# Kernel tuning notes

Hardware: AMD Instinct MI355X
Metric: run time of the kernel (lower is better)

Reference implementation:

```python
import jax, jax.numpy as jnp
import numpy as np
import math

N_EMBD = 1024
N_HEAD = 16
HEAD_SIZE = N_EMBD // N_HEAD
LAYER_IDX = 2
LAMBDA_INIT = 0.8 - 0.6 * math.exp(-0.3 * (LAYER_IDX - 1))
LN_EPS = 1e-5
B, T = 4, 1024


def setup_inputs() -> dict:
    key = jax.random.key(0)
    ks = jax.random.split(key, 11)
    s = 0.02  # weight init scale
    return {
        "x": jax.random.normal(ks[0], (B, T, N_EMBD), dtype=jnp.float32),
        "Wq1": jax.random.normal(ks[1], (N_EMBD, N_EMBD), dtype=jnp.float32) * s,
        "Wq2": jax.random.normal(ks[2], (N_EMBD, N_EMBD), dtype=jnp.float32) * s,
        "Wk1": jax.random.normal(ks[3], (N_EMBD, N_EMBD), dtype=jnp.float32) * s,
        "Wk2": jax.random.normal(ks[4], (N_EMBD, N_EMBD), dtype=jnp.float32) * s,
        "Wv": jax.random.normal(ks[5], (N_EMBD, 2 * N_EMBD), dtype=jnp.float32) * s,
        "Wc": jax.random.normal(ks[6], (2 * N_EMBD, N_EMBD), dtype=jnp.float32) * s,
        "lq1": jax.random.normal(ks[7], (N_HEAD, HEAD_SIZE), dtype=jnp.float32) * 0.1,
        "lk1": jax.random.normal(ks[8], (N_HEAD, HEAD_SIZE), dtype=jnp.float32) * 0.1,
        "lq2": jax.random.normal(ks[9], (N_HEAD, HEAD_SIZE), dtype=jnp.float32) * 0.1,
        "lk2": jax.random.normal(ks[10], (N_HEAD, HEAD_SIZE), dtype=jnp.float32) * 0.1,
    }


def reference(x, Wq1, Wq2, Wk1, Wk2, Wv, Wc, lq1, lk1, lq2, lk2):
    Bx, Tx, C = x.shape
    H, hs = N_HEAD, HEAD_SIZE
    scale = 1.0 / math.sqrt(hs)

    # projections -> (B, T, H, d)
    q1 = (x @ Wq1).reshape(Bx, Tx, H, hs)
    q2 = (x @ Wq2).reshape(Bx, Tx, H, hs)
    k1 = (x @ Wk1).reshape(Bx, Tx, H, hs)
    k2 = (x @ Wk2).reshape(Bx, Tx, H, hs)
    v = (x @ Wv).reshape(Bx, Tx, H, 2 * hs)

    # dual score streams (B, H, T, T)
    att1 = jnp.einsum("bqhd,bkhd->bhqk", q1, k1) * scale
    att2 = jnp.einsum("bqhd,bkhd->bhqk", q2, k2) * scale

    causal = jnp.tril(jnp.ones((Tx, Tx), dtype=bool))  # (T, T)
    neg_inf = jnp.float32(-jnp.inf)
    att1 = jnp.where(causal, att1, neg_inf)
    att2 = jnp.where(causal, att2, neg_inf)
    a1 = jax.nn.softmax(att1, axis=-1)
    a2 = jax.nn.softmax(att2, axis=-1)

    # per-head differential lambda
    lam1 = jnp.exp(jnp.sum(lq1 * lk1, axis=-1))  # (H,)
    lam2 = jnp.exp(jnp.sum(lq2 * lk2, axis=-1))  # (H,)
    lam_full = lam1 - lam2 + LAMBDA_INIT  # (H,)

    att = a1 - lam_full[None, :, None, None] * a2  # dropout = identity (eval)

    # PV matmul -> (B, T, H, 2*hs)
    y = jnp.einsum("bhqk,bkhd->bqhd", att, v)

    # subLN over last dim (no affine)
    mu = jnp.mean(y, axis=-1, keepdims=True)
    var = jnp.mean(jnp.square(y - mu), axis=-1, keepdims=True)
    y = (y - mu) / jnp.sqrt(var + LN_EPS)
    y = y * (1.0 - LAMBDA_INIT)

    y = y.reshape(Bx, Tx, 2 * C)
    return y @ Wc  # resid dropout = identity (eval)
```

## Files before the change

kernel.cpp:

```cpp
#include <hip/hip_runtime.h>


#define T_SEQ 1024
#define NH 16
#define DV 128
#define NPROJ 6144
#define KSTR 72

typedef __bf16 bf16_t;
typedef __bf16 bf16x8 __attribute__((ext_vector_type(8)));
typedef __bf16 bf16x4 __attribute__((ext_vector_type(4)));
typedef __bf16 bf16x2 __attribute__((ext_vector_type(2)));
typedef _Float16 f16x4 __attribute__((ext_vector_type(4)));
typedef _Float16 f16x2 __attribute__((ext_vector_type(2)));
typedef short s16x4 __attribute__((ext_vector_type(4)));
typedef float f32x4 __attribute__((ext_vector_type(4)));

#define LAMBDA_INIT 0.35550906759096928f
#define ONE_MINUS_LI 0.6444909324090307f
#define LOG2E 1.4426950408889634f
#define RTHR 44.36f

#if __has_builtin(__builtin_amdgcn_mfma_f32_16x16x16_bf16)
#define MFMA16(a, b, c) __builtin_amdgcn_mfma_f32_16x16x16_bf16(a, b, c, 0, 0, 0)
#elif __has_builtin(__builtin_amdgcn_mfma_f32_16x16x16bf16_1k)
#define MFMA16(a, b, c)                                                       \
  __builtin_amdgcn_mfma_f32_16x16x16bf16_1k(                                  \
      __builtin_bit_cast(s16x4, a), __builtin_bit_cast(s16x4, b), c, 0, 0, 0)
#else
#define MFMA16(a, b, c) (c)
#endif

#define MFMA32(a, b, c) __builtin_amdgcn_mfma_f32_16x16x32_bf16(a, b, c, 0, 0, 0)

#define GLDS(g, l)                                                            \
  __builtin_amdgcn_global_load_lds(                                           \
      (const __attribute__((address_space(1))) void*)(g),                     \
      (__attribute__((address_space(3))) void*)(l), 16, 0, 0)

static const size_t OFF_WCAT = 0;
static const size_t OFF_XB = OFF_WCAT + (size_t)6144 * 1024 * 2;
static const size_t OFF_WCT = OFF_XB + (size_t)4096 * 1024 * 2;
static const size_t OFF_PROJ = OFF_WCT + (size_t)2048 * 1024 * 2;
static const size_t OFF_VT = OFF_PROJ + (size_t)4096 * 6144 * 2;
static const size_t OFF_YLN = OFF_VT + (size_t)64 * 128 * 1024 * 2;
static const size_t OFF_LAM = OFF_YLN + (size_t)4096 * 2048 * 2;

__global__ void __launch_bounds__(256) cast_x(const float* __restrict__ x,
                                              bf16_t* __restrict__ o) {
  const int i = (blockIdx.x * 256 + threadIdx.x) * 4;
  float4 v = *(const float4*)(x + i);
  bf16x4 r = {(bf16_t)v.x, (bf16_t)v.y, (bf16_t)v.z, (bf16_t)v.w};
  *(bf16x4*)(o + i) = r;
}

__device__ __forceinline__ void tcast_body(const float* __restrict__ W,
                                           bf16_t* __restrict__ Wt, int K,
                                           int N, int row0) {
  __shared__ float tile[32][33];
  const int k0 = blockIdx.x * 32, n0 = blockIdx.y * 32;
  const int tx = threadIdx.x & 31, ty = threadIdx.x >> 5;
#pragma unroll
  for (int i = 0; i < 32; i += 8)
    tile[ty + i][tx] = W[(long)(k0 + ty + i) * N + n0 + tx];
  __syncthreads();
#pragma unroll
  for (int i = 0; i < 32; i += 8)
    Wt[(long)(row0 + n0 + ty + i) * K + k0 + tx] = (bf16_t)tile[tx][ty + i];
}

__global__ void __launch_bounds__(256) tcast_w(const float* __restrict__ W,
                                               bf16_t* __restrict__ Wt, int K,
                                               int N, int row0) {
  tcast_body(W, Wt, K, N, row0);
}

__global__ void __launch_bounds__(256) tcast_w4(const float* __restrict__ W0,
                                                const float* __restrict__ W1,
                                                const float* __restrict__ W2,
                                                const float* __restrict__ W3,
                                                bf16_t* __restrict__ Wt) {
  const float* Ws[4] = {W0, W1, W2, W3};
  tcast_body(Ws[blockIdx.z], Wt, 1024, 1024, blockIdx.z * 1024);
}

__global__ void lam_kernel(const float* __restrict__ lq1,
                           const float* __restrict__ lk1,
                           const float* __restrict__ lq2,
                           const float* __restrict__ lk2,
                           float* __restrict__ lam) {
  const int h = threadIdx.x;
  if (h < NH) {
    float d1 = 0.f, d2 = 0.f;
    for (int i = 0; i < 64; ++i) {
      d1 += lq1[h * 64 + i] * lk1[h * 64 + i];
      d2 += lq2[h * 64 + i] * lk2[h * 64 + i];
    }
    lam[h] = expf(d1) - expf(d2) + LAMBDA_INIT;
  }
}

#define GBM 256
#define GBN 256

#define GSTEP(tt, WAITSTR, DOPF)                                              \
  {                                                                           \
    asm volatile("s_waitcnt vmcnt(" WAITSTR ")" ::: "memory");                \
    __builtin_amdgcn_s_barrier();                                             \
    __builtin_amdgcn_sched_barrier(0);                                        \
    if (DOPF) {                                                               \
      const int sl_ = ((tt) + 3) & 3;                                         \
      const long ko_ = (long)((tt) + 3) * 32;                                 \
      GLDS(gA0 + ko_, &As[sl_][0] + tid * 8);                                 \
      GLDS(gA1 + ko_, &As[sl_][4096] + tid * 8);                              \
      GLDS(gB0 + ko_, &Bs[sl_][0] + tid * 8);                                 \
      GLDS(gB1 + ko_, &Bs[sl_][4096] + tid * 8);                              \
    }                                                                         \
    const int cs_ = (tt) & 3;                                                 \
    const bf16_t* Ab_ = &As[cs_][0] + arow_off;                               \
    const bf16_t* Bb_ = &Bs[cs_][0] + brow_off;                               \
    bf16x8 af_[8], bfv_[4];                                                   \
    _Pragma("unroll") for (int mt_ = 0; mt_ < 8; ++mt_)                       \
        af_[mt_] = *(const bf16x8*)(Ab_ + mt_ * 512);                         \
    _Pragma("unroll") for (int n_ = 0; n_ < 4; ++n_)                          \
        bfv_[n_] = *(const bf16x8*)(Bb_ + n_ * 512);                          \
    asm volatile("s_waitcnt lgkmcnt(0)" ::: "memory");                        \
    __builtin_amdgcn_sched_barrier(0);                                        \
    __builtin_amdgcn_s_setprio(1);                                            \
    _Pragma("unroll") for (int mt_ = 0; mt_ < 8; ++mt_)                       \
        _Pragma("unroll") for (int n_ = 0; n_ < 4; ++n_)                      \
            acc[mt_][n_] = MFMA32(af_[mt_], bfv_[n_], acc[mt_][n_]);          \
    __builtin_amdgcn_s_setprio(0);                                            \
  }

__global__ void __launch_bounds__(512, 1) gemm256(const bf16_t* __restrict__ A,
                                                  const bf16_t* __restrict__ Bt,
                                                  bf16_t* __restrict__ C,
                                                  int M, int N, int K,
                                                  int nbx) {
  __shared__ __align__(16) bf16_t As[4][GBM * 32];
  __shared__ __align__(16) bf16_t Bs[4][GBN * 32];
  const int tid = threadIdx.x;
  const int w = tid >> 6, lane = tid & 63;
  const int quad = lane >> 4, l16 = lane & 15;
  const int wr = w >> 2, wc = w & 3;

  const int wg = blockIdx.x;
  const int cpx = gridDim.x >> 3;
  const int sw = (wg & 7) * cpx + (wg >> 3);
  const int by = sw / nbx, bx = sw % nbx;
  const int m0 = by * GBM, n0 = bx * GBN;

  const int srow = tid >> 2;
  const int scol = (tid & 3) * 8;
  const bf16_t* gA0 = A + (long)(m0 + srow) * K + scol;
  const bf16_t* gA1 = gA0 + (long)128 * K;
  const bf16_t* gB0 = Bt + (long)(n0 + srow) * K + scol;
  const bf16_t* gB1 = gB0 + (long)128 * K;

  const int arow_off = (wr * 128 + l16) * 32 + quad * 8;
  const int brow_off = (wc * 64 + l16) * 32 + quad * 8;

  f32x4 acc[8][4] = {};
  const int nsteps = K >> 5;

#pragma unroll
  for (int c = 0; c < 3; ++c) {
    GLDS(gA0 + c * 32, &As[c][0] + tid * 8);
    GLDS(gA1 + c * 32, &As[c][4096] + tid * 8);
    GLDS(gB0 + c * 32, &Bs[c][0] + tid * 8);
    GLDS(gB1 + c * 32, &Bs[c][4096] + tid * 8);
  }

  for (int t = 0; t + 3 < nsteps; ++t) GSTEP(t, "8", 1);
  GSTEP(nsteps - 3, "8", 0);
  GSTEP(nsteps - 2, "4", 0);
  GSTEP(nsteps - 1, "0", 0);

#pragma unroll
  for (int mt = 0; mt < 8; ++mt)
#pragma unroll
    for (int n = 0; n < 4; ++n) {
      const int col = n0 + wc * 64 + n * 16 + l16;
#pragma unroll
      for (int i = 0; i < 4; ++i) {
        const int row = m0 + wr * 128 + mt * 16 + quad * 4 + i;
        C[(long)row * N + col] = (bf16_t)acc[mt][n][i];
      }
    }
}

#define BM 128
#define BK 32

template <typename OutT>
__global__ void __launch_bounds__(256) gemm_bt_n64(const bf16_t* __restrict__ A,
                                                   const bf16_t* __restrict__ Bt,
                                                   OutT* __restrict__ C, int M,
                                                   int N, int K) {
  __shared__ __align__(16) bf16_t As[BM * BK];
  __shared__ __align__(16) bf16_t Bs[64 * BK];
  const int tid = threadIdx.x;
  const int w = tid >> 6;
  const int lane = tid & 63;
  const int quad = lane >> 4, l16 = lane & 15;
  const int m0 = blockIdx.y * BM, n0 = blockIdx.x * 64;
  const int wm = (w >> 1) * 64, wn = (w & 1) * 32;
  const int srow = tid >> 2;
  const int scol = (tid & 3) * 8;

  const bf16_t* Ag0 = A + (long)(m0 + srow) * K + scol;
  const bf16_t* Ag1 = Ag0 + (long)64 * K;
  const bf16_t* Bg0 = Bt + (long)(n0 + srow) * K + scol;
  bf16_t* lA0 = As + tid * 8;
  bf16_t* lA1 = As + 2048 + tid * 8;
  bf16_t* lB0 = Bs + tid * 8;

  f32x4 acc[4][2] = {};

  for (int k0 = 0; k0 < K; k0 += BK) {
    GLDS(Ag0 + k0, lA0);
    GLDS(Ag1 + k0, lA1);
    GLDS(Bg0 + k0, lB0);
    __syncthreads();
    bf16x8 af[4], bfr[2];
#pragma unroll
    for (int t = 0; t < 4; ++t)
      af[t] = *(const bf16x8*)(As + (wm + t * 16 + l16) * BK + quad * 8);
#pragma unroll
    for (int t = 0; t < 2; ++t)
      bfr[t] = *(const bf16x8*)(Bs + (wn + t * 16 + l16) * BK + quad * 8);
#pragma unroll
    for (int mt = 0; mt < 4; ++mt)
#pragma unroll
      for (int ntt = 0; ntt < 2; ++ntt)
        acc[mt][ntt] = MFMA32(af[mt], bfr[ntt], acc[mt][ntt]);
    __syncthreads();
  }

#pragma unroll
  for (int mt = 0; mt < 4; ++mt)
#pragma unroll
    for (int ntt = 0; ntt < 2; ++ntt) {
      const int col = n0 + wn + ntt * 16 + l16;
#pragma unroll
      for (int i = 0; i < 4; ++i) {
        const int row = m0 + wm + mt * 16 + quad * 4 + i;
        C[(long)row * N + col] = (OutT)acc[mt][ntt][i];
      }
    }
}

__global__ void __launch_bounds__(256) transpose_v(const bf16_t* __restrict__ proj,
                                                   bf16_t* __restrict__ vt) {
  __shared__ bf16_t tile[32][34];
  const int bh = blockIdx.z;
  const int b = bh >> 4, h = bh & 15;
  const int t0 = blockIdx.x * 32, d0 = blockIdx.y * 32;
  const int tx = threadIdx.x & 31, ty = threadIdx.x >> 5;
  const bf16_t* src = proj + (long)(b * T_SEQ) * NPROJ + 4096 + h * 128;
#pragma unroll
  for (int i = 0; i < 32; i += 8)
    tile[ty + i][tx] = src[(long)(t0 + ty + i) * NPROJ + d0 + tx];
  __syncthreads();
  const int d_loc = threadIdx.x >> 3;
  const int g = threadIdx.x & 7;
  const int s = g >> 2, qd = g & 3;
  const int tl = s * 16 + qd * 4;
  bf16x4 o = {tile[tl + 0][d_loc], tile[tl + 1][d_loc], tile[tl + 2][d_loc],
              tile[tl + 3][d_loc]};
  bf16_t* dst = vt + (long)bh * (DV * T_SEQ) + (long)(d0 + d_loc) * T_SEQ;
  *(bf16x4*)(dst + t0 + qd * 8 + s * 4) = o;
}

__global__ void __launch_bounds__(256) attn_kernel(const bf16_t* __restrict__ proj,
                                                   const bf16_t* __restrict__ vt,
                                                   _Float16* __restrict__ a1,
                                                   _Float16* __restrict__ a2) {
  const int x = blockIdx.x;
  const int p = x >> 7;
  const int st = (x >> 6) & 1;
  const int bh = x & 63;
  const int b = bh >> 4, h = bh & 15;
  const int tid = threadIdx.x;
  const int w = tid >> 6, lane = tid & 63;
  const int quad = lane >> 4, l16 = lane & 15;
  const long bT = (long)b * T_SEQ;

  __shared__ __align__(16) bf16_t Ks[64 * KSTR];
  __shared__ __align__(16) bf16_t Vs[DV * KSTR];

  const int koff = h * 64 + 2048 + st * 1024;
  const bf16_t* gK = proj + (bT + (tid >> 2)) * (long)NPROJ + koff + (tid & 3) * 16;
  const bf16_t* gV = vt + (long)bh * DV * T_SEQ + (long)(tid >> 1) * T_SEQ +
                     (tid & 1) * 32;
  const int kwK = (tid >> 2) * KSTR + (tid & 3) * 16;
  const int kwV = (tid >> 1) * KSTR + (tid & 1) * 32;

  const float sc = 0.125f * LOG2E;
  const bf16x4 one4 = {(bf16_t)1.0f, (bf16_t)1.0f, (bf16_t)1.0f, (bf16_t)1.0f};

  for (int ph = 0; ph < 2; ++ph) {
    const int qblk = ph ? p : 15 - p;
    const int q0 = qblk * 64 + w * 16;
    const int qg = q0 + l16;

    const bf16_t* qrow = proj + (bT + qg) * (long)NPROJ + h * 64 + st * 1024;
    bf16x8 aq[2];
    aq[0] = *(const bf16x8*)(qrow + quad * 8);
    aq[1] = *(const bf16x8*)(qrow + 32 + quad * 8);

    f32x4 O[8] = {};
    float m = -3.0e38f, l = 0.f;

    const int kend_blk = qblk * 64 + 64;
    const int kend_w = q0 + 16;

    bf16x8 rK[2], rV[4];
    rK[0] = *(const bf16x8*)(gK);
    rK[1] = *(const bf16x8*)(gK + 8);
#pragma unroll
    for (int j = 0; j < 4; ++j) rV[j] = *(const bf16x8*)(gV + j * 8);

    for (int kt = 0; kt < kend_blk; kt += 64) {
      *(bf16x8*)(Ks + kwK) = rK[0];
      *(bf16x8*)(Ks + kwK + 8) = rK[1];
#pragma unroll
      for (int j = 0; j < 4; ++j) *(bf16x8*)(Vs + kwV + j * 8) = rV[j];
      __syncthreads();

      if (kt + 64 < kend_blk) {
        const long ko = (long)(kt + 64) * NPROJ;
        rK[0] = *(const bf16x8*)(gK + ko);
        rK[1] = *(const bf16x8*)(gK + ko + 8);
#pragma unroll
        for (int j = 0; j < 4; ++j)
          rV[j] = *(const bf16x8*)(gV + kt + 64 + j * 8);
      }

      if (kt < kend_w) {
        f32x4 s[4];
#pragma unroll
        for (int c = 0; c < 4; ++c) {
          const bf16_t* kr = Ks + (c * 16 + l16) * KSTR;
          bf16x8 ka0 = *(const bf16x8*)(kr + quad * 8);
          bf16x8 ka1 = *(const bf16x8*)(kr + 32 + quad * 8);
          f32x4 z = {};
          z = MFMA32(ka0, aq[0], z);
          z = MFMA32(ka1, aq[1], z);
          s[c] = z;
        }
        if (kt + 63 > q0) {
#pragma unroll
          for (int c = 0; c < 4; ++c)
#pragma unroll
            for (int i = 0; i < 4; ++i) {
              const int key = kt + c * 16 + quad * 4 + i;
              if (key > qg) s[c][i] = -1e30f;
            }
        }
        float t[4];
#pragma unroll
        for (int c = 0; c < 4; ++c)
          t[c] = fmaxf(fmaxf(s[c][0], s[c][1]), fmaxf(s[c][2], s[c][3]));
        float mx = fmaxf(fmaxf(t[0], t[1]), fmaxf(t[2], t[3]));
        mx = fmaxf(mx, __shfl_xor(mx, 16));
        mx = fmaxf(mx, __shfl_xor(mx, 32));
        if (!__all(mx <= m + RTHR)) {
          const float mn = fmaxf(m, mx);
          const float al = exp2f((m - mn) * sc);
          m = mn;
#pragma unroll
          for (int f = 0; f < 8; ++f)
#pragma unroll
            for (int i = 0; i < 4; ++i) O[f][i] *= al;
          l *= al;
        }
        const float ms = m * sc;
        bf16x4 pc[4];
#pragma unroll
        for (int c = 0; c < 4; ++c)
#pragma unroll
          for (int i = 0; i < 4; ++i)
            pc[c][i] = (bf16_t)exp2f(fmaf(s[c][i], sc, -ms));
        f32x4 la = {};
#pragma unroll
        for (int c = 0; c < 4; ++c) la = MFMA16(one4, pc[c], la);
#pragma unroll
        for (int cp = 0; cp < 2; ++cp) {
#pragma unroll
          for (int f = 0; f < 8; ++f) {
            bf16x8 va = *(const bf16x8*)(Vs + (f * 16 + l16) * KSTR +
                                         cp * 32 + quad * 8);
            bf16x4 lo = __builtin_shufflevector(va, va, 0, 1, 2, 3);
            bf16x4 hi = __builtin_shufflevector(va, va, 4, 5, 6, 7);
            O[f] = MFMA16(lo, pc[2 * cp], O[f]);
            O[f] = MFMA16(hi, pc[2 * cp + 1], O[f]);
          }
        }
        l += la[0];
      }
      __syncthreads();
    }

    const float inv = 1.0f / l;
    _Float16* ob = st ? a2 : a1;
    _Float16* dst = ob + ((bT + qg) * 16 + h) * (long)128 + quad * 4;
#pragma unroll
    for (int f = 0; f < 8; ++f) {
      f16x4 o = {(_Float16)(O[f][0] * inv), (_Float16)(O[f][1] * inv),
                 (_Float16)(O[f][2] * inv), (_Float16)(O[f][3] * inv)};
      *(f16x4*)(dst + f * 16) = o;
    }
  }
}

__global__ void __launch_bounds__(256) combine_kernel(const _Float16* __restrict__ a1,
                                                      const _Float16* __restrict__ a2,
                                                      const float* __restrict__ lamp,
                                                      bf16_t* __restrict__ yln) {
  const int unit = blockIdx.x * 4 + (threadIdx.x >> 6);
  const int lane = threadIdx.x & 63;
  const float lam = lamp[unit & 15];
  const long base = (long)unit * 128 + lane * 2;
  f16x2 v1 = *(const f16x2*)(a1 + base);
  f16x2 v2 = *(const f16x2*)(a2 + base);
  float y0 = (float)v1[0] - lam * (float)v2[0];
  float y1 = (float)v1[1] - lam * (float)v2[1];
  float sm = y0 + y1, sq = y0 * y0 + y1 * y1;
#pragma unroll
  for (int off = 1; off < 64; off <<= 1) {
    sm += __shfl_xor(sm, off);
    sq += __shfl_xor(sq, off);
  }
  const float mu = sm * (1.0f / 128.0f);
  const float var = sq * (1.0f / 128.0f) - mu * mu;
  const float rs = rsqrtf(var + 1e-5f) * ONE_MINUS_LI;
  bf16x2 o = {(bf16_t)((y0 - mu) * rs), (bf16_t)((y1 - mu) * rs)};
  *(bf16x2*)(yln + base) = o;
}

extern "C" void kernel_launch(void* const* d_in, const int* in_sizes, int n_in,
                              void* d_out, int out_size, void* d_ws,
                              size_t ws_size, hipStream_t stream) {
  const float* x = (const float*)d_in[0];
  const float* Wq1 = (const float*)d_in[1];
  const float* Wq2 = (const float*)d_in[2];
  const float* Wk1 = (const float*)d_in[3];
  const float* Wk2 = (const float*)d_in[4];
  const float* Wv = (const float*)d_in[5];
  const float* Wc = (const float*)d_in[6];
  const float* lq1 = (const float*)d_in[7];
  const float* lk1 = (const float*)d_in[8];
  const float* lq2 = (const float*)d_in[9];
  const float* lk2 = (const float*)d_in[10];
  float* out = (float*)d_out;

  char* ws = (char*)d_ws;
  bf16_t* wcat = (bf16_t*)(ws + OFF_WCAT);
  bf16_t* xb = (bf16_t*)(ws + OFF_XB);
  bf16_t* wct = (bf16_t*)(ws + OFF_WCT);
  bf16_t* projb = (bf16_t*)(ws + OFF_PROJ);
  bf16_t* vtb = (bf16_t*)(ws + OFF_VT);
  bf16_t* ylnb = (bf16_t*)(ws + OFF_YLN);
  float* lamp = (float*)(ws + OFF_LAM);
  _Float16* a1b = (_Float16*)(ws + OFF_YLN);
  _Float16* a2b = (_Float16*)(ws + OFF_WCAT);

  cast_x<<<4096, 256, 0, stream>>>(x, xb);
  tcast_w4<<<dim3(32, 32, 4), 256, 0, stream>>>(Wq1, Wq2, Wk1, Wk2, wcat);
  tcast_w<<<dim3(32, 64), 256, 0, stream>>>(Wv, wcat, 1024, 2048, 4096);
  tcast_w<<<dim3(64, 32), 256, 0, stream>>>(Wc, wct, 2048, 1024, 0);
  lam_kernel<<<1, 64, 0, stream>>>(lq1, lk1, lq2, lk2, lamp);

  gemm256<<<dim3(384), 512, 0, stream>>>(xb, wcat, projb, 4096, 6144, 1024, 24);
  transpose_v<<<dim3(32, 4, 64), 256, 0, stream>>>(projb, vtb);
  attn_kernel<<<dim3(1024), 256, 0, stream>>>(projb, vtb, a1b, a2b);
  combine_kernel<<<dim3(16384), 256, 0, stream>>>(a1b, a2b, lamp, ylnb);
  gemm_bt_n64<float><<<dim3(16, 32), 256, 0, stream>>>(ylnb, wct, out, 4096, 1024, 2048);
}
```

Measured before the change: 327.0 us.

## Restructure projection GEMM to 256x128x64 tiles with swizzled LDS and split-stage pipeline

Rewrites the main projection GEMM to use 256x128 output tiles with a K-step of 64, doubling the grid to 768 blocks. Global-to-LDS loads go into two buffers with an XOR swizzle on the column chunk, which is meant to avoid LDS bank conflicts. Each K step is split into two half-stages so the loads for the next step overlap the MFMAs of the current one. The smaller N tile increases A-tile reloads but gives more blocks to fill the CUs, and the hand-tuned vmcnt counts must stay correct.

```diff
diff --git a/kernel.cpp b/kernel.cpp
--- a/kernel.cpp
+++ b/kernel.cpp
@@ -101,36 +101,26 @@
 }
 
 #define GBM 256
-#define GBN 256
-
-#define GSTEP(tt, WAITSTR, DOPF)                                              \
+#define GBN 128
+#define GBK 64
+
+#define STAGE_S0(buf, tt)                                                     \
   {                                                                           \
-    asm volatile("s_waitcnt vmcnt(" WAITSTR ")" ::: "memory");                \
-    __builtin_amdgcn_s_barrier();                                             \
-    __builtin_amdgcn_sched_barrier(0);                                        \
-    if (DOPF) {                                                               \
-      const int sl_ = ((tt) + 3) & 3;                                         \
-      const long ko_ = (long)((tt) + 3) * 32;                                 \
-      GLDS(gA0 + ko_, &As[sl_][0] + tid * 8);                                 \
-      GLDS(gA1 + ko_, &As[sl_][4096] + tid * 8);                              \
-      GLDS(gB0 + ko_, &Bs[sl_][0] + tid * 8);                                 \
-      GLDS(gB1 + ko_, &Bs[sl_][4096] + tid * 8);                              \
-    }                                                                         \
-    const int cs_ = (tt) & 3;                                                 \
-    const bf16_t* Ab_ = &As[cs_][0] + arow_off;                               \
-    const bf16_t* Bb_ = &Bs[cs_][0] + brow_off;                               \
-    bf16x8 af_[8], bfv_[4];                                                   \
-    _Pragma("unroll") for (int mt_ = 0; mt_ < 8; ++mt_)                       \
-        af_[mt_] = *(const bf16x8*)(Ab_ + mt_ * 512);                         \
-    _Pragma("unroll") for (int n_ = 0; n_ < 4; ++n_)                          \
-        bfv_[n_] = *(const bf16x8*)(Bb_ + n_ * 512);                          \
-    asm volatile("s_waitcnt lgkmcnt(0)" ::: "memory");                        \
-    __builtin_amdgcn_sched_barrier(0);                                        \
-    __builtin_amdgcn_s_setprio(1);                                            \
-    _Pragma("unroll") for (int mt_ = 0; mt_ < 8; ++mt_)                       \
-        _Pragma("unroll") for (int n_ = 0; n_ < 4; ++n_)                      \
-            acc[mt_][n_] = MFMA32(af_[mt_], bfv_[n_], acc[mt_][n_]);          \
-    __builtin_amdgcn_s_setprio(0);                                            \
+    const long kk_ = (long)(tt)*GBK;                                          \
+    GLDS(gA + kk_, (bf16_t*)((char*)As[buf] + tid * 16));                     \
+    GLDS(gA + (long)128 * K + kk_,                                            \
+         (bf16_t*)((char*)As[buf] + 16384 + tid * 16));                       \
+    GLDS(gB + kk_, (bf16_t*)((char*)Bs[buf] + tid * 16));                     \
+    GLDS(gB + (long)64 * K + kk_,                                             \
+         (bf16_t*)((char*)Bs[buf] + 8192 + tid * 16));                        \
+  }
+#define STAGE_S1(buf, tt)                                                     \
+  {                                                                           \
+    const long kk_ = (long)(tt)*GBK;                                          \
+    GLDS(gA + (long)64 * K + kk_,                                             \
+         (bf16_t*)((char*)As[buf] + 8192 + tid * 16));                        \
+    GLDS(gA + (long)192 * K + kk_,                                            \
+         (bf16_t*)((char*)As[buf] + 24576 + tid * 16));                       \
   }
 
 __global__ void __launch_bounds__(512, 1) gemm256(const bf16_t* __restrict__ A,
@@ -138,8 +128,8 @@
                                                   bf16_t* __restrict__ C,
                                                   int M, int N, int K,
                                                   int nbx) {
-  __shared__ __align__(16) bf16_t As[4][GBM * 32];
-  __shared__ __align__(16) bf16_t Bs[4][GBN * 32];
+  __shared__ __align__(16) bf16_t As[2][GBM * GBK];
+  __shared__ __align__(16) bf16_t Bs[2][GBN * GBK];
   const int tid = threadIdx.x;
   const int w = tid >> 6, lane = tid & 63;
   const int quad = lane >> 4, l16 = lane & 15;
@@ -151,42 +141,95 @@
   const int by = sw / nbx, bx = sw % nbx;
   const int m0 = by * GBM, n0 = bx * GBN;
 
-  const int srow = tid >> 2;
-  const int scol = (tid & 3) * 8;
-  const bf16_t* gA0 = A + (long)(m0 + srow) * K + scol;
-  const bf16_t* gA1 = gA0 + (long)128 * K;
-  const bf16_t* gB0 = Bt + (long)(n0 + srow) * K + scol;
-  const bf16_t* gB1 = gB0 + (long)128 * K;
-
-  const int arow_off = (wr * 128 + l16) * 32 + quad * 8;
-  const int brow_off = (wc * 64 + l16) * 32 + quad * 8;
-
-  f32x4 acc[8][4] = {};
-  const int nsteps = K >> 5;
-
-#pragma unroll
-  for (int c = 0; c < 3; ++c) {
-    GLDS(gA0 + c * 32, &As[c][0] + tid * 8);
-    GLDS(gA1 + c * 32, &As[c][4096] + tid * 8);
-    GLDS(gB0 + c * 32, &Bs[c][0] + tid * 8);
-    GLDS(gB1 + c * 32, &Bs[c][4096] + tid * 8);
-  }
-
-  for (int t = 0; t + 3 < nsteps; ++t) GSTEP(t, "8", 1);
-  GSTEP(nsteps - 3, "8", 0);
-  GSTEP(nsteps - 2, "4", 0);
-  GSTEP(nsteps - 1, "0", 0);
-
-#pragma unroll
-  for (int mt = 0; mt < 8; ++mt)
-#pragma unroll
-    for (int n = 0; n < 4; ++n) {
-      const int col = n0 + wc * 64 + n * 16 + l16;
-#pragma unroll
-      for (int i = 0; i < 4; ++i) {
-        const int row = m0 + wr * 128 + mt * 16 + quad * 4 + i;
-        C[(long)row * N + col] = (bf16_t)acc[mt][n][i];
+  const int rp = tid >> 3;
+  const int gsrc = ((tid & 7) ^ (rp & 7)) * 8;
+  const bf16_t* gA = A + (long)(m0 + rp) * K + gsrc;
+  const bf16_t* gB = Bt + (long)(n0 + rp) * K + gsrc;
+
+  const int sx = l16 & 7;
+  const int ko0 = (quad ^ sx) * 16;
+  const int ko1 = ((4 + quad) ^ sx) * 16;
+
+  f32x4 acc[8][2] = {};
+  const int ntk = K >> 6;
+
+  STAGE_S0(0, 0);
+  STAGE_S1(0, 0);
+  STAGE_S0(1, 1);
+  asm volatile("s_waitcnt vmcnt(6)" ::: "memory");
+  __builtin_amdgcn_s_barrier();
+  __builtin_amdgcn_sched_barrier(0);
+
+  for (int t = 0; t < ntk; ++t) {
+    const int cur = t & 1, nxt = cur ^ 1;
+    const char* Ab = (const char*)As[cur] + (size_t)(wr * 128 + l16) * 128;
+    const char* Bb = (const char*)Bs[cur] + (size_t)(wc * 32 + l16) * 128;
+
+    if (t > 0 && t + 1 < ntk) STAGE_S0(nxt, t + 1);
+    bf16x8 af[4][2], bfv[2][2];
+#pragma unroll
+    for (int mt = 0; mt < 4; ++mt) {
+      af[mt][0] = *(const bf16x8*)(Ab + (size_t)mt * 2048 + ko0);
+      af[mt][1] = *(const bf16x8*)(Ab + (size_t)mt * 2048 + ko1);
+    }
+#pragma unroll
+    for (int n = 0; n < 2; ++n) {
+      bfv[n][0] = *(const bf16x8*)(Bb + (size_t)n * 2048 + ko0);
+      bfv[n][1] = *(const bf16x8*)(Bb + (size_t)n * 2048 + ko1);
+    }
+    asm volatile("s_waitcnt lgkmcnt(0)" ::: "memory");
+    __builtin_amdgcn_sched_barrier(0);
+    __builtin_amdgcn_s_setprio(1);
+#pragma unroll
+    for (int mt = 0; mt < 4; ++mt)
+#pragma unroll
+      for (int n = 0; n < 2; ++n) {
+        acc[mt][n] = MFMA32(af[mt][0], bfv[n][0], acc[mt][n]);
+        acc[mt][n] = MFMA32(af[mt][1], bfv[n][1], acc[mt][n]);
       }
+    __builtin_amdgcn_s_setprio(0);
+    if (t + 1 < ntk) {
+      asm volatile("s_waitcnt vmcnt(4)" ::: "memory");
+    } else {
+      asm volatile("s_waitcnt vmcnt(0)" ::: "memory");
+    }
+    __builtin_amdgcn_s_barrier();
+    __builtin_amdgcn_sched_barrier(0);
+
+    if (t + 1 < ntk) STAGE_S1(nxt, t + 1);
+    bf16x8 ag[4][2];
+#pragma unroll
+    for (int mt = 0; mt < 4; ++mt) {
+      ag[mt][0] = *(const bf16x8*)(Ab + 8192 + (size_t)mt * 2048 + ko0);
+      ag[mt][1] = *(const bf16x8*)(Ab + 8192 + (size_t)mt * 2048 + ko1);
+    }
+    asm volatile("s_waitcnt lgkmcnt(0)" ::: "memory");
+    __builtin_amdgcn_sched_barrier(0);
+    __builtin_amdgcn_s_setprio(1);
+#pragma unroll
+    for (int mt = 0; mt < 4; ++mt)
+#pragma unroll
+      for (int n = 0; n < 2; ++n) {
+        acc[4 + mt][n] = MFMA32(ag[mt][0], bfv[n][0], acc[4 + mt][n]);
+        acc[4 + mt][n] = MFMA32(ag[mt][1], bfv[n][1], acc[4 + mt][n]);
+      }
+    __builtin_amdgcn_s_setprio(0);
+    if (t + 1 < ntk) {
+      asm volatile("s_waitcnt vmcnt(2)" ::: "memory");
+    }
+    __builtin_amdgcn_s_barrier();
+    __builtin_amdgcn_sched_barrier(0);
+  }
+
+#pragma unroll
+  for (int am = 0; am < 8; ++am)
+#pragma unroll
+    for (int n = 0; n < 2; ++n) {
+      const int col = n0 + wc * 32 + n * 16 + l16;
+      const int rbase = m0 + wr * 128 + (am >> 2) * 64 + (am & 3) * 16 + quad * 4;
+#pragma unroll
+      for (int i = 0; i < 4; ++i)
+        C[(long)(rbase + i) * N + col] = (bf16_t)acc[am][n][i];
     }
 }
 
@@ -473,7 +516,7 @@
   tcast_w<<<dim3(64, 32), 256, 0, stream>>>(Wc, wct, 2048, 1024, 0);
   lam_kernel<<<1, 64, 0, stream>>>(lq1, lk1, lq2, lk2, lamp);
 
-  gemm256<<<dim3(384), 512, 0, stream>>>(xb, wcat, projb, 4096, 6144, 1024, 24);
+  gemm256<<<dim3(768), 512, 0, stream>>>(xb, wcat, projb, 4096, 6144, 1024, 48);
   transpose_v<<<dim3(32, 4, 64), 256, 0, stream>>>(projb, vtb);
   attn_kernel<<<dim3(1024), 256, 0, stream>>>(projb, vtb, a1b, a2b);
   combine_kernel<<<dim3(16384), 256, 0, stream>>>(a1b, a2b, lamp, ylnb);
```

New measurement: 333.2 us. Within noise of the previous version (+1.9%).
